# Kernel optimization log

Hardware: AMD Instinct MI355X
Metric: run time of the kernel (lower is better)

## Reference

```python
import jax, jax.numpy as jnp
import numpy as np

B, D, E, H, K = 8192, 1024, 8, 4096, 2

def setup_inputs() -> dict:
    key = jax.random.key(0)
    ks = jax.random.split(key, 7)
    s_in = 1.0 / np.sqrt(D)
    s_hid = 1.0 / np.sqrt(H)
    return {
        "z":  jax.random.normal(ks[0], (B, D), dtype=jnp.float32),
        "Wg": jax.random.uniform(ks[1], (D, E), jnp.float32, -s_in, s_in),
        "bg": jnp.zeros((E,), jnp.float32),
        "W1": jax.random.uniform(ks[2], (E, D, H), jnp.float32, -s_in, s_in),
        "b1": jax.random.uniform(ks[3], (E, H), jnp.float32, -s_in, s_in),
        "W2": jax.random.uniform(ks[4], (E, H, D), jnp.float32, -s_hid, s_hid),
        "b2": jax.random.uniform(ks[5], (E, D), jnp.float32, -s_hid, s_hid),
    }

def reference(z, Wg, bg, W1, b1, W2, b2):
    # gate: softmax over experts, then keep only top-k weights (no renorm,
    # matching the original which sums topw * expert(z))
    w = jax.nn.softmax(z @ Wg + bg, axis=-1)            # [B, E]
    topw, idx = jax.lax.top_k(w, K)                      # [B, K] each
    wmask = jnp.zeros_like(w).at[jnp.arange(B)[:, None], idx].set(topw)  # [B, E]
    # dense all-expert MLP, then weighted combine (same math as per-token loop)
    h = jax.nn.relu(jnp.einsum('bd,edh->beh', z, W1) + b1)   # [B, E, H]
    y = jnp.einsum('beh,ehd->bed', h, W2) + b2               # [B, E, D]
    out = jnp.einsum('be,bed->bd', wmask, y)                 # [B, D]
    return out
```

## Files before the change

kernel.cpp:

```cpp
#include <hip/hip_runtime.h>
#include <hip/hip_bf16.h>
#include <cstdint>
#include <cstddef>

#define BTOK  8192
#define DIM   1024
#define NEXP  8
#define NHID  4096
#define HHALF 2048
#define GATE_TOK 64
#define ABASE (128 * 32)

typedef __bf16 bf16x8 __attribute__((ext_vector_type(8)));
typedef float  floatx4 __attribute__((ext_vector_type(4)));

#define O_COUNTS 0
#define O_BASE   256
#define O_TOKB   1024
#define O_TOKW   (O_TOKB + (size_t)NEXP*BTOK*4)
#define O_CE     (O_TOKW + (size_t)NEXP*BTOK*4)
#define O_CP     (O_CE + (size_t)2*BTOK*4)
#define O_CW     (O_CP + (size_t)2*BTOK*4)
#define O_ZBF    (O_CW + (size_t)2*BTOK*4)
#define O_W1T    (O_ZBF + (size_t)BTOK*DIM*2)
#define O_W2T    (O_W1T + (size_t)NEXP*DIM*NHID*2)
#define O_HBUF   (O_W2T + (size_t)NEXP*DIM*NHID*2)
#define WS_BASE  (O_HBUF + (size_t)2*BTOK*HHALF*2)

__device__ __forceinline__ void gload_lds16(const void* g, void* l) {
  __builtin_amdgcn_global_load_lds(
      (const __attribute__((address_space(1))) void*)g,
      (__attribute__((address_space(3))) void*)l, 16, 0, 0);
}

__device__ __forceinline__ ushort f2bf(float x) {
  return __builtin_bit_cast(ushort, __float2bfloat16(x));
}

__global__ void k_zcnt(int* __restrict__ counts) {
  if (threadIdx.x < 12) counts[threadIdx.x] = 0;
}

__global__ void k_zout(float* __restrict__ out) {
  int i = blockIdx.x * blockDim.x + threadIdx.x;
  float4 z4 = {0.f, 0.f, 0.f, 0.f};
  float4* o = (float4*)out;
  int n = BTOK * DIM / 4;
  for (int j = i; j < n; j += gridDim.x * blockDim.x) o[j] = z4;
}

__global__ __launch_bounds__(256) void k_transpose(
    const float* __restrict__ src, __hip_bfloat16* __restrict__ dst, int R, int C) {
  __shared__ float tile[32][33];
  int zz = blockIdx.z;
  const float* s = src + (size_t)zz * R * C;
  __hip_bfloat16* d = dst + (size_t)zz * R * C;
  int c0 = blockIdx.x * 32, r0 = blockIdx.y * 32;
  int tx = threadIdx.x & 31, ty = threadIdx.x >> 5;
#pragma unroll
  for (int i = ty; i < 32; i += 8)
    tile[i][tx] = s[(size_t)(r0 + i) * C + c0 + tx];
  __syncthreads();
#pragma unroll
  for (int i = ty; i < 32; i += 8)
    d[(size_t)(c0 + i) * R + r0 + tx] = __float2bfloat16(tile[tx][i]);
}

__global__ __launch_bounds__(256) void k_gate(
    const float* __restrict__ z, const float* __restrict__ Wg,
    const float* __restrict__ bg, int* __restrict__ counts,
    int* __restrict__ tokb, float* __restrict__ tokw,
    __hip_bfloat16* __restrict__ zbf) {
  __shared__ float wgT[NEXP * DIM];
  __shared__ int   le[2 * GATE_TOK];
  __shared__ float lw[2 * GATE_TOK];
  __shared__ int   lr[2 * GATE_TOK];
  __shared__ int   lcnt[NEXP];
  __shared__ int   gbase[NEXP];

  int tid = threadIdx.x;
  if (tid < NEXP) lcnt[tid] = 0;
#pragma unroll
  for (int e = 0; e < NEXP; e++)
    for (int d = tid; d < DIM; d += 256)
      wgT[e * DIM + d] = Wg[d * NEXP + e];
  __syncthreads();

  int lane = tid & 63;
  int wv = tid >> 6;
  int b0 = blockIdx.x * GATE_TOK;

  for (int t = 0; t < 16; t++) {
    int lt = wv * 16 + t;
    int b = b0 + lt;
    const float4* zr4 = (const float4*)(z + (size_t)b * DIM);
    float4 zv[4];
#pragma unroll
    for (int i = 0; i < 4; i++) zv[i] = zr4[lane + 64 * i];
    ushort4* zb4 = (ushort4*)((ushort*)zbf + (size_t)b * DIM);
#pragma unroll
    for (int i = 0; i < 4; i++) {
      ushort4 u;
      u.x = f2bf(zv[i].x); u.y = f2bf(zv[i].y);
      u.z = f2bf(zv[i].z); u.w = f2bf(zv[i].w);
      zb4[lane + 64 * i] = u;
    }
    float acc[NEXP];
#pragma unroll
    for (int e = 0; e < NEXP; e++) acc[e] = 0.f;
#pragma unroll
    for (int e = 0; e < NEXP; e++) {
      const float4* wg4 = (const float4*)(wgT + e * DIM);
#pragma unroll
      for (int i = 0; i < 4; i++) {
        float4 w4 = wg4[lane + 64 * i];
        acc[e] += zv[i].x * w4.x + zv[i].y * w4.y + zv[i].z * w4.z + zv[i].w * w4.w;
      }
    }
#pragma unroll
    for (int off = 32; off > 0; off >>= 1) {
#pragma unroll
      for (int e = 0; e < NEXP; e++) acc[e] += __shfl_down(acc[e], off);
    }
    if (lane == 0) {
      float mx = -1e30f;
#pragma unroll
      for (int e = 0; e < NEXP; e++) { acc[e] += bg[e]; mx = fmaxf(mx, acc[e]); }
      float s = 0.f;
#pragma unroll
      for (int e = 0; e < NEXP; e++) { acc[e] = expf(acc[e] - mx); s += acc[e]; }
      float inv = 1.f / s;
      int i1 = -1, i2 = -1; float v1 = -1.f, v2 = -1.f;
#pragma unroll
      for (int e = 0; e < NEXP; e++) {
        float w = acc[e] * inv;
        if (w > v1) { v2 = v1; i2 = i1; v1 = w; i1 = e; }
        else if (w > v2) { v2 = w; i2 = e; }
      }
      le[2 * lt] = i1;     lw[2 * lt] = v1;
      le[2 * lt + 1] = i2; lw[2 * lt + 1] = v2;
    }
  }
  __syncthreads();
  if (tid < 2 * GATE_TOK) lr[tid] = atomicAdd(&lcnt[le[tid]], 1);
  __syncthreads();
  if (tid < NEXP) gbase[tid] = atomicAdd(&counts[tid], lcnt[tid]);
  __syncthreads();
  if (tid < 2 * GATE_TOK) {
    int e = le[tid];
    int p = gbase[e] + lr[tid];
    int b = b0 + (tid >> 1);
    tokb[e * BTOK + p] = b;
    tokw[e * BTOK + p] = lw[tid];
  }
}

__global__ void k_base(const int* __restrict__ counts, int* __restrict__ base) {
  if (threadIdx.x == 0 && blockIdx.x == 0) {
    int s = 0;
    for (int e = 0; e < NEXP; e++) { base[e] = s; s += counts[e]; }
    int a = 0, b = 0;
    base[8] = 0; base[17] = 0;
    for (int e = 0; e < NEXP; e++) {
      int mt = (counts[e] + 127) >> 7;
      a += mt * 8; b += mt * 4;
      base[9 + e] = a; base[18 + e] = b;
    }
  }
}


#define STG3(nxt_, tt_) do {                                                 \
    gload_lds16(srcA  + (tt_) * 32, &lds[nxt_][(wv * 16) * 32]);             \
    gload_lds16(srcB0 + (tt_) * 32, &lds[nxt_][ABASE + (wv * 16) * 32]);     \
    gload_lds16(srcB1 + (tt_) * 32, &lds[nxt_][ABASE + (128 + wv * 16) * 32]);\
  } while (0)

#define PH3(cur_, STG_, VM_) do {                                            \
    const ushort* Ab_ = &lds[cur_][0];                                       \
    const ushort* Bb_ = &lds[cur_][ABASE];                                   \
    bf16x8 afr_[4], bfr_[4];                                                 \
    _Pragma("unroll")                                                        \
    for (int j_ = 0; j_ < 4; j_++)                                           \
      bfr_[j_] = __builtin_bit_cast(bf16x8,                                  \
          *(const uint4*)(Bb_ + boff + j_ * 512));                           \
    _Pragma("unroll")                                                        \
    for (int i_ = 0; i_ < 4; i_++)                                           \
      afr_[i_] = __builtin_bit_cast(bf16x8,                                  \
          *(const uint4*)(Ab_ + aoff + i_ * 512));                           \
    STG_;                                                                    \
    __builtin_amdgcn_sched_barrier(0);                                       \
    VM_;                                                                     \
    __builtin_amdgcn_s_barrier();                                            \
    __builtin_amdgcn_sched_barrier(0);                                       \
    __builtin_amdgcn_s_setprio(1);                                           \
    _Pragma("unroll")                                                        \
    for (int i_ = 0; i_ < 4; i_++)                                           \
      _Pragma("unroll")                                                      \
      for (int j_ = 0; j_ < 4; j_++)                                         \
        acc[i_][j_] = __builtin_amdgcn_mfma_f32_16x16x32_bf16(               \
            afr_[i_], bfr_[j_], acc[i_][j_], 0, 0, 0);                       \
    __builtin_amdgcn_s_setprio(0);                                           \
    __builtin_amdgcn_sched_barrier(0);                                       \
    __builtin_amdgcn_s_barrier();                                            \
  } while (0)

#define VM3  asm volatile("s_waitcnt vmcnt(3)" ::: "memory")
#define VM0  asm volatile("s_waitcnt vmcnt(0)" ::: "memory")
#define NOP_ (void)0

__global__ __launch_bounds__(512, 4) void k_gemm1(
    const __hip_bfloat16* __restrict__ zbf, const __hip_bfloat16* __restrict__ w1t,
    const float* __restrict__ b1, const int* __restrict__ counts,
    const int* __restrict__ base, const int* __restrict__ tokb,
    __hip_bfloat16* __restrict__ hbuf, int hbase,
    const int* __restrict__ tp, int* __restrict__ steal) {
  __shared__ __align__(16) ushort lds[3][(128 + 256) * 32];
  __shared__ int sh_g;

  int tid = threadIdx.x;
  int lane = tid & 63;
  int wv = tid >> 6;
  int wm = wv >> 2;
  int wn = wv & 3;
  int lrow = lane & 15;
  int quad = lane >> 4;
  int pc = quad ^ ((lrow >> 1) & 3);
  int aoff = (wm * 64 + lrow) * 32 + pc * 8;
  int boff = (wn * 64 + lrow) * 32 + pc * 8;
  int srow = wv * 16 + (lane >> 2);
  int sswz = ((lane & 3) ^ ((srow >> 1) & 3)) * 8;

  const ushort* zb = (const ushort*)zbf;
  const ushort* w1 = (const ushort*)w1t;
  const int NT = DIM / 32;
  int TT = tp[8];

  for (;;) {
    if (tid == 0) sh_g = atomicAdd(steal, 1);
    __syncthreads();
    int g = sh_g;
    if (g >= TT) break;

    int e = 0;
    while (g >= tp[e + 1]) e++;
    int local = g - tp[e];
    int mte = (tp[e + 1] - tp[e]) >> 3;
    int nt = local / mte;
    int mtl = local - nt * mte;
    int m0 = mtl * 128, n0 = nt * 256;
    int cnt = counts[e], gb = base[e];

    int m = m0 + srow; if (m >= cnt) m = cnt - 1;
    const ushort* srcA = zb + (size_t)tokb[e * BTOK + m] * DIM + sswz;
    const ushort* srcB0 = w1 + (size_t)(e * NHID + hbase + n0 + srow) * DIM + sswz;
    const ushort* srcB1 = w1 + (size_t)(e * NHID + hbase + n0 + 128 + srow) * DIM + sswz;

    STG3(0, 0);
    STG3(1, 1);
    VM3;
    __builtin_amdgcn_s_barrier();

    floatx4 acc[4][4];
#pragma unroll
    for (int i = 0; i < 4; i++)
#pragma unroll
      for (int j = 0; j < 4; j++) { floatx4 zf = {0.f,0.f,0.f,0.f}; acc[i][j] = zf; }

    int cur = 0;
#pragma unroll 1
    for (int t = 0; t < NT - 2; ++t) {
      int nxt = cur + 2; if (nxt >= 3) nxt -= 3;
      PH3(cur, STG3(nxt, t + 2), VM3);
      cur = (cur == 2) ? 0 : cur + 1;
    }
    PH3(cur, NOP_, VM0);
    cur = (cur == 2) ? 0 : cur + 1;
    PH3(cur, NOP_, NOP_);

    float bias[4];
#pragma unroll
    for (int j = 0; j < 4; j++)
      bias[j] = b1[e * NHID + hbase + n0 + wn * 64 + j * 16 + lrow];
    ushort* hp = (ushort*)hbuf;
#pragma unroll
    for (int i = 0; i < 4; i++) {
      int mloc = wm * 64 + i * 16 + quad * 4;
#pragma unroll
      for (int r = 0; r < 4; r++) {
        int mm = m0 + mloc + r;
        if (mm < cnt) {
          ushort* hr = hp + (size_t)(gb + mm) * HHALF;
#pragma unroll
          for (int j = 0; j < 4; j++) {
            float v = fmaxf(acc[i][j][r] + bias[j], 0.f);
            hr[n0 + wn * 64 + j * 16 + lrow] = f2bf(v);
          }
        }
      }
    }
    __syncthreads();
  }
}

__global__ __launch_bounds__(512, 4) void k_gemm2(
    const __hip_bfloat16* __restrict__ hbuf, const __hip_bfloat16* __restrict__ w2t,
    const float* __restrict__ b2, const int* __restrict__ counts,
    const int* __restrict__ base, const int* __restrict__ tokb,
    const float* __restrict__ tokw, float* __restrict__ out,
    int hbase, int pass, const int* __restrict__ tp) {
  __shared__ __align__(16) ushort lds[3][(128 + 256) * 32];

  int tid = threadIdx.x;
  int lane = tid & 63;
  int wv = tid >> 6;
  int wm = wv >> 2;
  int wn = wv & 3;
  int lrow = lane & 15;
  int quad = lane >> 4;
  int pc = quad ^ ((lrow >> 1) & 3);
  int aoff = (wm * 64 + lrow) * 32 + pc * 8;
  int boff = (wn * 64 + lrow) * 32 + pc * 8;
  int srow = wv * 16 + (lane >> 2);
  int sswz = ((lane & 3) ^ ((srow >> 1) & 3)) * 8;

  const ushort* hb = (const ushort*)hbuf;
  const ushort* w2 = (const ushort*)w2t;
  const int NT = HHALF / 32;

  int TT = tp[8];
  int totalU = TT * NT;
  int q = (totalU + (int)gridDim.x - 1) / (int)gridDim.x;
  int u  = (int)blockIdx.x * q;
  int u1 = u + q; if (u1 > totalU) u1 = totalU;

  while (u < u1) {
    int g = u / NT;
    int ks0 = u - g * NT;
    int nk = NT - ks0;
    if (nk > u1 - u) nk = u1 - u;

    int e = 0;
    while (g >= tp[e + 1]) e++;
    int local = g - tp[e];
    int mte = (tp[e + 1] - tp[e]) >> 2;
    int nt = local / mte;
    int mtl = local - nt * mte;
    int m0 = mtl * 128, n0 = nt * 256;
    int cnt = counts[e], gb = base[e];

    int m = m0 + srow; if (m >= cnt) m = cnt - 1;
    const ushort* srcA = hb + (size_t)(gb + m) * HHALF + sswz;
    const ushort* srcB0 = w2 + (size_t)(e * DIM + n0 + srow) * NHID + hbase + sswz;
    const ushort* srcB1 = w2 + (size_t)(e * DIM + n0 + 128 + srow) * NHID + hbase + sswz;

    STG3(0, ks0);
    if (nk > 1) { STG3(1, ks0 + 1); VM3; }
    else        { VM0; }
    __builtin_amdgcn_s_barrier();

    floatx4 acc[4][4];
#pragma unroll
    for (int i = 0; i < 4; i++)
#pragma unroll
      for (int j = 0; j < 4; j++) { floatx4 zf = {0.f,0.f,0.f,0.f}; acc[i][j] = zf; }

    int cur = 0;
#pragma unroll 1
    for (int t = 0; t < nk - 2; ++t) {
      int nxt = cur + 2; if (nxt >= 3) nxt -= 3;
      PH3(cur, STG3(nxt, ks0 + t + 2), VM3);
      cur = (cur == 2) ? 0 : cur + 1;
    }
    if (nk > 1) {
      PH3(cur, NOP_, VM0);
      cur = (cur == 2) ? 0 : cur + 1;
    }
    PH3(cur, NOP_, NOP_);

    bool addb2 = (pass == 0) && (ks0 == 0);
#pragma unroll
    for (int i = 0; i < 4; i++) {
      int mloc = wm * 64 + i * 16 + quad * 4;
#pragma unroll
      for (int r = 0; r < 4; r++) {
        int mm = m0 + mloc + r;
        if (mm < cnt) {
          int tk  = tokb[e * BTOK + mm];
          float w = tokw[e * BTOK + mm];
#pragma unroll
          for (int j = 0; j < 4; j++) {
            int n = n0 + wn * 64 + j * 16 + lrow;
            float v = acc[i][j][r] + (addb2 ? b2[e * DIM + n] : 0.f);
            atomicAdd(&out[(size_t)tk * DIM + n], w * v);
          }
        }
      }
    }
    u += nk;
  }
}

extern "C" void kernel_launch(void* const* d_in, const int* in_sizes, int n_in,
                              void* d_out, int out_size, void* d_ws, size_t ws_size,
                              hipStream_t stream) {
  const float* z  = (const float*)d_in[0];
  const float* Wg = (const float*)d_in[1];
  const float* bg = (const float*)d_in[2];
  const float* W1 = (const float*)d_in[3];
  const float* b1 = (const float*)d_in[4];
  const float* W2 = (const float*)d_in[5];
  const float* b2 = (const float*)d_in[6];
  float* out = (float*)d_out;
  char* ws = (char*)d_ws;
  if (ws_size < WS_BASE) return;

  int*   counts = (int*)(ws + O_COUNTS);
  int*   base   = (int*)(ws + O_BASE);
  int*   tokb   = (int*)(ws + O_TOKB);
  float* tokw   = (float*)(ws + O_TOKW);
  __hip_bfloat16* zbf  = (__hip_bfloat16*)(ws + O_ZBF);
  __hip_bfloat16* w1t  = (__hip_bfloat16*)(ws + O_W1T);
  __hip_bfloat16* w2t  = (__hip_bfloat16*)(ws + O_W2T);
  __hip_bfloat16* hbuf = (__hip_bfloat16*)(ws + O_HBUF);

  k_zcnt<<<1, 64, 0, stream>>>(counts);
  k_zout<<<512, 256, 0, stream>>>(out);
  k_transpose<<<dim3(NHID / 32, DIM / 32, NEXP), 256, 0, stream>>>(W1, w1t, DIM, NHID);
  k_transpose<<<dim3(DIM / 32, NHID / 32, NEXP), 256, 0, stream>>>(W2, w2t, NHID, DIM);
  k_gate<<<BTOK / GATE_TOK, 256, 0, stream>>>(z, Wg, bg, counts, tokb, tokw, zbf);
  k_base<<<1, 64, 0, stream>>>(counts, base);
  for (int half = 0; half < 2; half++) {
    k_gemm1<<<512, 512, 0, stream>>>(
        zbf, w1t, b1, counts, base, tokb, hbuf, half * HHALF,
        base + 8, counts + 8 + half * 2);
    k_gemm2<<<512, 512, 0, stream>>>(
        hbuf, w2t, b2, counts, base, tokb, tokw, out,
        half * HHALF, half, base + 17);
  }
}
```

Before: 1.005 ms.

## Merge two hidden-half passes into single GEMM1/GEMM2 launches with work stealing

Replaces the two-pass loop over hidden halves with one GEMM1 launch covering the full hidden dimension, writing into a full-width hidden buffer. GEMM2 moves from static split-K partitioning to atomic work stealing over (tile, K-half) units, and the bias is added only on the first K segment. This removes two kernel launches and their tail effects and aims to balance load dynamically. In exchange the hidden buffer doubles in size, since its offset now reserves 2*BTOK*NHID entries, which raises the workspace requirement. The steal counters at counts+8 and counts+9 are zeroed by the existing counter-reset kernel.

Measured after the change: 879.3 us. 12.5% less time.

```diff
diff --git a/kernel.cpp b/kernel.cpp
--- a/kernel.cpp
+++ b/kernel.cpp
@@ -25,7 +25,7 @@
 #define O_W1T    (O_ZBF + (size_t)BTOK*DIM*2)
 #define O_W2T    (O_W1T + (size_t)NEXP*DIM*NHID*2)
 #define O_HBUF   (O_W2T + (size_t)NEXP*DIM*NHID*2)
-#define WS_BASE  (O_HBUF + (size_t)2*BTOK*HHALF*2)
+#define WS_NEED  (O_HBUF + (size_t)2*BTOK*NHID*2)
 
 __device__ __forceinline__ void gload_lds16(const void* g, void* l) {
   __builtin_amdgcn_global_load_lds(
@@ -163,7 +163,7 @@
     base[8] = 0; base[17] = 0;
     for (int e = 0; e < NEXP; e++) {
       int mt = (counts[e] + 127) >> 7;
-      a += mt * 8; b += mt * 4;
+      a += mt * 16; b += mt * 4;
       base[9 + e] = a; base[18 + e] = b;
     }
   }
@@ -213,7 +213,7 @@
     const __hip_bfloat16* __restrict__ zbf, const __hip_bfloat16* __restrict__ w1t,
     const float* __restrict__ b1, const int* __restrict__ counts,
     const int* __restrict__ base, const int* __restrict__ tokb,
-    __hip_bfloat16* __restrict__ hbuf, int hbase,
+    __hip_bfloat16* __restrict__ hbuf,
     const int* __restrict__ tp, int* __restrict__ steal) {
   __shared__ __align__(16) ushort lds[3][(128 + 256) * 32];
   __shared__ int sh_g;
@@ -245,7 +245,7 @@
     int e = 0;
     while (g >= tp[e + 1]) e++;
     int local = g - tp[e];
-    int mte = (tp[e + 1] - tp[e]) >> 3;
+    int mte = (tp[e + 1] - tp[e]) >> 4;
     int nt = local / mte;
     int mtl = local - nt * mte;
     int m0 = mtl * 128, n0 = nt * 256;
@@ -253,8 +253,8 @@
 
     int m = m0 + srow; if (m >= cnt) m = cnt - 1;
     const ushort* srcA = zb + (size_t)tokb[e * BTOK + m] * DIM + sswz;
-    const ushort* srcB0 = w1 + (size_t)(e * NHID + hbase + n0 + srow) * DIM + sswz;
-    const ushort* srcB1 = w1 + (size_t)(e * NHID + hbase + n0 + 128 + srow) * DIM + sswz;
+    const ushort* srcB0 = w1 + (size_t)(e * NHID + n0 + srow) * DIM + sswz;
+    const ushort* srcB1 = w1 + (size_t)(e * NHID + n0 + 128 + srow) * DIM + sswz;
 
     STG3(0, 0);
     STG3(1, 1);
@@ -281,7 +281,7 @@
     float bias[4];
 #pragma unroll
     for (int j = 0; j < 4; j++)
-      bias[j] = b1[e * NHID + hbase + n0 + wn * 64 + j * 16 + lrow];
+      bias[j] = b1[e * NHID + n0 + wn * 64 + j * 16 + lrow];
     ushort* hp = (ushort*)hbuf;
 #pragma unroll
     for (int i = 0; i < 4; i++) {
@@ -290,7 +290,7 @@
       for (int r = 0; r < 4; r++) {
         int mm = m0 + mloc + r;
         if (mm < cnt) {
-          ushort* hr = hp + (size_t)(gb + mm) * HHALF;
+          ushort* hr = hp + (size_t)(gb + mm) * NHID;
 #pragma unroll
           for (int j = 0; j < 4; j++) {
             float v = fmaxf(acc[i][j][r] + bias[j], 0.f);
@@ -308,8 +308,9 @@
     const float* __restrict__ b2, const int* __restrict__ counts,
     const int* __restrict__ base, const int* __restrict__ tokb,
     const float* __restrict__ tokw, float* __restrict__ out,
-    int hbase, int pass, const int* __restrict__ tp) {
+    const int* __restrict__ tp, int* __restrict__ steal) {
   __shared__ __align__(16) ushort lds[3][(128 + 256) * 32];
+  __shared__ int sh_g;
 
   int tid = threadIdx.x;
   int lane = tid & 63;
@@ -327,18 +328,15 @@
   const ushort* hb = (const ushort*)hbuf;
   const ushort* w2 = (const ushort*)w2t;
   const int NT = HHALF / 32;
-
   int TT = tp[8];
-  int totalU = TT * NT;
-  int q = (totalU + (int)gridDim.x - 1) / (int)gridDim.x;
-  int u  = (int)blockIdx.x * q;
-  int u1 = u + q; if (u1 > totalU) u1 = totalU;
-
-  while (u < u1) {
-    int g = u / NT;
-    int ks0 = u - g * NT;
-    int nk = NT - ks0;
-    if (nk > u1 - u) nk = u1 - u;
+
+  for (;;) {
+    if (tid == 0) sh_g = atomicAdd(steal, 1);
+    __syncthreads();
+    int gu = sh_g;
+    if (gu >= 2 * TT) break;
+    int g = gu >> 1;
+    int kseg = gu & 1;
 
     int e = 0;
     while (g >= tp[e + 1]) e++;
@@ -350,13 +348,13 @@
     int cnt = counts[e], gb = base[e];
 
     int m = m0 + srow; if (m >= cnt) m = cnt - 1;
-    const ushort* srcA = hb + (size_t)(gb + m) * HHALF + sswz;
-    const ushort* srcB0 = w2 + (size_t)(e * DIM + n0 + srow) * NHID + hbase + sswz;
-    const ushort* srcB1 = w2 + (size_t)(e * DIM + n0 + 128 + srow) * NHID + hbase + sswz;
-
-    STG3(0, ks0);
-    if (nk > 1) { STG3(1, ks0 + 1); VM3; }
-    else        { VM0; }
+    const ushort* srcA = hb + (size_t)(gb + m) * NHID + kseg * HHALF + sswz;
+    const ushort* srcB0 = w2 + (size_t)(e * DIM + n0 + srow) * NHID + kseg * HHALF + sswz;
+    const ushort* srcB1 = w2 + (size_t)(e * DIM + n0 + 128 + srow) * NHID + kseg * HHALF + sswz;
+
+    STG3(0, 0);
+    STG3(1, 1);
+    VM3;
     __builtin_amdgcn_s_barrier();
 
     floatx4 acc[4][4];
@@ -367,18 +365,15 @@
 
     int cur = 0;
 #pragma unroll 1
-    for (int t = 0; t < nk - 2; ++t) {
+    for (int t = 0; t < NT - 2; ++t) {
       int nxt = cur + 2; if (nxt >= 3) nxt -= 3;
-      PH3(cur, STG3(nxt, ks0 + t + 2), VM3);
+      PH3(cur, STG3(nxt, t + 2), VM3);
       cur = (cur == 2) ? 0 : cur + 1;
     }
-    if (nk > 1) {
-      PH3(cur, NOP_, VM0);
-      cur = (cur == 2) ? 0 : cur + 1;
-    }
+    PH3(cur, NOP_, VM0);
+    cur = (cur == 2) ? 0 : cur + 1;
     PH3(cur, NOP_, NOP_);
 
-    bool addb2 = (pass == 0) && (ks0 == 0);
 #pragma unroll
     for (int i = 0; i < 4; i++) {
       int mloc = wm * 64 + i * 16 + quad * 4;
@@ -391,13 +386,13 @@
 #pragma unroll
           for (int j = 0; j < 4; j++) {
             int n = n0 + wn * 64 + j * 16 + lrow;
-            float v = acc[i][j][r] + (addb2 ? b2[e * DIM + n] : 0.f);
+            float v = acc[i][j][r] + (kseg == 0 ? b2[e * DIM + n] : 0.f);
             atomicAdd(&out[(size_t)tk * DIM + n], w * v);
           }
         }
       }
     }
-    u += nk;
+    __syncthreads();
   }
 }
 
@@ -413,7 +408,7 @@
   const float* b2 = (const float*)d_in[6];
   float* out = (float*)d_out;
   char* ws = (char*)d_ws;
-  if (ws_size < WS_BASE) return;
+  if (ws_size < WS_NEED) return;
 
   int*   counts = (int*)(ws + O_COUNTS);
   int*   base   = (int*)(ws + O_BASE);
@@ -430,12 +425,8 @@
   k_transpose<<<dim3(DIM / 32, NHID / 32, NEXP), 256, 0, stream>>>(W2, w2t, NHID, DIM);
   k_gate<<<BTOK / GATE_TOK, 256, 0, stream>>>(z, Wg, bg, counts, tokb, tokw, zbf);
   k_base<<<1, 64, 0, stream>>>(counts, base);
-  for (int half = 0; half < 2; half++) {
-    k_gemm1<<<512, 512, 0, stream>>>(
-        zbf, w1t, b1, counts, base, tokb, hbuf, half * HHALF,
-        base + 8, counts + 8 + half * 2);
-    k_gemm2<<<512, 512, 0, stream>>>(
-        hbuf, w2t, b2, counts, base, tokb, tokw, out,
-        half * HHALF, half, base + 17);
-  }
-}
+  k_gemm1<<<512, 512, 0, stream>>>(
+      zbf, w1t, b1, counts, base, tokb, hbuf, base + 8, counts + 8);
+  k_gemm2<<<512, 512, 0, stream>>>(
+      hbuf, w2t, b2, counts, base, tokb, tokw, out, base + 17, counts + 9);
+}
```
